# Kernel tuning notes

Hardware: AMD Instinct MI355X
Metric: run time of the kernel (lower is better)

The kernel has to match this reference:

```python
import jax, jax.numpy as jnp
import numpy as np

D_MODEL = 1024
NUM_HEADS = 16
DEPTH = D_MODEL // NUM_HEADS
NEG_INF_SCALE = -1e9


def setup_inputs() -> dict:
    key = jax.random.key(0)
    ks = jax.random.split(key, 12)
    B, S = 2, 2048
    q = jax.random.normal(ks[0], (B, S, D_MODEL), dtype=jnp.float32)
    k = jax.random.normal(ks[1], (B, S, D_MODEL), dtype=jnp.float32)
    v = jax.random.normal(ks[2], (B, S, D_MODEL), dtype=jnp.float32)
    # causal mask: 1 where attention is disallowed (future positions)
    mask = jnp.triu(jnp.ones((S, S), dtype=jnp.float32), k=1)[None, None]
    scale = 1.0 / np.sqrt(D_MODEL)
    Wq = jax.random.normal(ks[3], (D_MODEL, D_MODEL), dtype=jnp.float32) * scale
    bq = jnp.zeros((D_MODEL,), dtype=jnp.float32)
    Wk = jax.random.normal(ks[4], (D_MODEL, D_MODEL), dtype=jnp.float32) * scale
    bk = jnp.zeros((D_MODEL,), dtype=jnp.float32)
    Wv = jax.random.normal(ks[5], (D_MODEL, D_MODEL), dtype=jnp.float32) * scale
    bv = jnp.zeros((D_MODEL,), dtype=jnp.float32)
    Wo = jax.random.normal(ks[6], (D_MODEL, D_MODEL), dtype=jnp.float32) * scale
    bo = jnp.zeros((D_MODEL,), dtype=jnp.float32)
    return {"v": v, "k": k, "q": q, "mask": mask,
            "Wq": Wq, "bq": bq, "Wk": Wk, "bk": bk,
            "Wv": Wv, "bv": bv, "Wo": Wo, "bo": bo}


def _split_heads(x):
    B, S, _ = x.shape
    return x.reshape(B, S, NUM_HEADS, DEPTH).transpose(0, 2, 1, 3)  # [B,H,S,depth]


def reference(v, k, q, mask, Wq, bq, Wk, bk, Wv, bv, Wo, bo):
    B, Sq, _ = q.shape
    qh = _split_heads(q @ Wq + bq)  # [B,H,Sq,depth]
    kh = _split_heads(k @ Wk + bk)  # [B,H,Sk,depth]
    vh = _split_heads(v @ Wv + bv)  # [B,H,Sk,depth]
    logits = jnp.einsum('bhqd,bhkd->bhqk', qh, kh) / jnp.sqrt(
        jnp.asarray(DEPTH, dtype=jnp.float32))
    logits = logits + mask * NEG_INF_SCALE
    attn = jax.nn.softmax(logits, axis=-1)
    out = jnp.einsum('bhqk,bhkd->bhqd', attn, vh)  # [B,H,Sq,depth]
    out = out.transpose(0, 2, 1, 3).reshape(B, Sq, D_MODEL)
    return out @ Wo + bo
```

## Files before the change

### kernel.cpp

```cpp
#include <hip/hip_runtime.h>
#include <stdint.h>

#define D_MODEL 1024
#define NHEADS  16
#define DEPTH   64
#define BATCH   2
#define SEQ     2048
#define M_TOT   (BATCH * SEQ)

#define Q_SCALE 0.18033688011112042f

typedef unsigned short u16;
typedef unsigned int   u32;
typedef __attribute__((ext_vector_type(8))) short bf16x8;
typedef __attribute__((ext_vector_type(4))) float f32x4;

__device__ __forceinline__ float bf2f(unsigned int u) {
    union { unsigned int i; float f; } x;
    x.i = (u & 0xffffu) << 16;
    return x.f;
}
__device__ __forceinline__ u16 f2bf(float f) {
    union { float f; unsigned int i; } x;
    x.f = f;
    unsigned int lsb = (x.i >> 16) & 1u;
    x.i += 0x7fffu + lsb;
    return (u16)(x.i >> 16);
}
__device__ __forceinline__ u32 fbits(float f) {
    union { float f; unsigned int i; } x; x.f = f; return x.i;
}
__device__ __forceinline__ float exp2f_hw(float x) {
    return __builtin_amdgcn_exp2f(x);
}

template <int CTRL>
__device__ __forceinline__ float dppf(float x) {
    int r = __builtin_amdgcn_update_dpp(0, (int)fbits(x), CTRL, 0xF, 0xF, false);
    union { int i; float f; } u; u.i = r; return u.f;
}
__device__ __forceinline__ float redmax16(float x) {
    x = fmaxf(x, dppf<0xB1>(x));
    x = fmaxf(x, dppf<0x4E>(x));
    x = fmaxf(x, dppf<0x124>(x));
    x = fmaxf(x, dppf<0x128>(x));
    return x;
}
__device__ __forceinline__ float redsum16(float x) {
    x += dppf<0xB1>(x);
    x += dppf<0x4E>(x);
    x += dppf<0x124>(x);
    x += dppf<0x128>(x);
    return x;
}

__device__ __forceinline__ void stage16(const u16* g, u16* ldsbase) {
#if __has_builtin(__builtin_amdgcn_global_load_lds)
    __builtin_amdgcn_global_load_lds(
        (const __attribute__((address_space(1))) unsigned int*)g,
        (__attribute__((address_space(3))) unsigned int*)ldsbase, 16, 0, 0);
#else
    int lane = threadIdx.x & 63;
    *(uint4*)(ldsbase + lane * 8) = *(const uint4*)g;
#endif
}

__global__ void sniff_kernel(const u16* __restrict__ q, int* __restrict__ flag) {
    const int t = threadIdx.x;
    int cnt = 0;
    #pragma unroll
    for (int j = 0; j < 4; ++j) {
        unsigned int bits = q[2 * (t + 64 * j)];
        bool susp = ((bits & 0x7fffu) >= 0x4780u);
        cnt += (int)__popcll(__ballot(susp));
    }
    if (t == 0) flag[0] = (cnt >= 32) ? 1 : 0;
}

__global__ __launch_bounds__(256)
void wT_kernel(const void* W0, const void* W1, const void* W2, const void* W3,
               u16* T0, u16* T1, u16* T2, u16* T3, const int* __restrict__ flag) {
    __shared__ u16 t[64][72];
    const int z = blockIdx.z;
    const void* Wv = (z == 0) ? W0 : (z == 1) ? W1 : (z == 2) ? W2 : W3;
    u16* WT = (z == 0) ? T0 : (z == 1) ? T1 : (z == 2) ? T2 : T3;
    const int f32 = *flag;
    const int tid = threadIdx.x;
    const int n0 = blockIdx.x * 64, k0 = blockIdx.y * 64;

    #pragma unroll
    for (int cb = 0; cb < 2; ++cb) {
        int c = tid + cb * 256;
        int kl = c >> 3, nc = (c & 7) * 8;
        size_t off = (size_t)(k0 + kl) * D_MODEL + n0 + nc;
        u16 tmp[8];
        if (f32) {
            const float* W = (const float*)Wv;
            float4 a = *(const float4*)(W + off);
            float4 b = *(const float4*)(W + off + 4);
            tmp[0] = f2bf(a.x); tmp[1] = f2bf(a.y); tmp[2] = f2bf(a.z); tmp[3] = f2bf(a.w);
            tmp[4] = f2bf(b.x); tmp[5] = f2bf(b.y); tmp[6] = f2bf(b.z); tmp[7] = f2bf(b.w);
        } else {
            *(uint4*)tmp = *(const uint4*)((const u16*)Wv + off);
        }
        *(uint4*)&t[kl][nc] = *(uint4*)tmp;
    }
    __syncthreads();
    #pragma unroll
    for (int cb = 0; cb < 2; ++cb) {
        int c = tid + cb * 256;
        int nl = c >> 3, kc = (c & 7) * 8;
        u16 tmp[8];
        #pragma unroll
        for (int i = 0; i < 8; ++i) tmp[i] = t[kc + i][nl];
        *(uint4*)(WT + (size_t)(n0 + nl) * D_MODEL + k0 + kc) = *(uint4*)tmp;
    }
}

struct GemmJob {
    const void* A;
    const u16*  BT;
    const void* bias;
    void*       C;
    int a_ext;
    int cmode;
    float scale;
};

__global__ __launch_bounds__(256)
void gemm5(GemmJob j0, GemmJob j1, GemmJob j2, const int* __restrict__ flag) {
    __shared__ u16 Als[128 * 64];
    __shared__ u16 Bls[128 * 64];
    GemmJob jb = (blockIdx.z == 0) ? j0 : (blockIdx.z == 1) ? j1 : j2;

    const int f32 = *flag;
    const int af32 = jb.a_ext & f32;
    const int tid = threadIdx.x;
    const int w = tid >> 6, lane = tid & 63;
    const int cc = lane & 15, quad = lane >> 4;
    const int wm = w >> 1, wn = w & 1;
    const int m0 = blockIdx.y * 128, n0 = blockIdx.x * 128;

    f32x4 zero4 = {0.f, 0.f, 0.f, 0.f};
    f32x4 acc[4][4];
    #pragma unroll
    for (int i = 0; i < 4; ++i)
        #pragma unroll
        for (int j = 0; j < 4; ++j) acc[i][j] = zero4;

    const int srow_off = lane >> 3;
    const int sg8 = ((lane & 7) ^ ((lane >> 3) & 7)) * 8;

    for (int k0 = 0; k0 < D_MODEL; k0 += 64) {
        __syncthreads();
        #pragma unroll
        for (int i = 0; i < 4; ++i) {
            int c = w * 4 + i;
            int row = c * 8 + srow_off;
            stage16(jb.BT + (size_t)(n0 + row) * D_MODEL + k0 + sg8, &Bls[c * 512]);
        }
        if (!af32) {
            const u16* A = (const u16*)jb.A;
            #pragma unroll
            for (int i = 0; i < 4; ++i) {
                int c = w * 4 + i;
                int row = c * 8 + srow_off;
                stage16(A + (size_t)(m0 + row) * D_MODEL + k0 + sg8, &Als[c * 512]);
            }
        } else {
            const float* A = (const float*)jb.A;
            #pragma unroll
            for (int c2 = 0; c2 < 4; ++c2) {
                int row = c2 * 32 + (tid >> 3);
                int gg = tid & 7;
                int lg = (gg ^ (row & 7)) * 8;
                const float* gp = A + (size_t)(m0 + row) * D_MODEL + k0 + gg * 8;
                float4 a = *(const float4*)gp;
                float4 b = *(const float4*)(gp + 4);
                u16 t8[8];
                t8[0] = f2bf(a.x); t8[1] = f2bf(a.y); t8[2] = f2bf(a.z); t8[3] = f2bf(a.w);
                t8[4] = f2bf(b.x); t8[5] = f2bf(b.y); t8[6] = f2bf(b.z); t8[7] = f2bf(b.w);
                *(uint4*)&Als[row * 64 + lg] = *(uint4*)t8;
            }
        }
        __syncthreads();

        const int sw = cc & 7;
        bf16x8 af[4][2], bf[4][2];
        #pragma unroll
        for (int i = 0; i < 4; ++i) {
            const u16* ar = &Als[(wm * 64 + i * 16 + cc) * 64];
            af[i][0] = *(const bf16x8*)(ar + ((quad ^ sw) * 8));
            af[i][1] = *(const bf16x8*)(ar + (((4 + quad) ^ sw) * 8));
        }
        #pragma unroll
        for (int j = 0; j < 4; ++j) {
            const u16* br = &Bls[(wn * 64 + j * 16 + cc) * 64];
            bf[j][0] = *(const bf16x8*)(br + ((quad ^ sw) * 8));
            bf[j][1] = *(const bf16x8*)(br + (((4 + quad) ^ sw) * 8));
        }
        #pragma unroll
        for (int i = 0; i < 4; ++i)
            #pragma unroll
            for (int j = 0; j < 4; ++j) {
                acc[i][j] = __builtin_amdgcn_mfma_f32_16x16x32_bf16(af[i][0], bf[j][0], acc[i][j], 0, 0, 0);
                acc[i][j] = __builtin_amdgcn_mfma_f32_16x16x32_bf16(af[i][1], bf[j][1], acc[i][j], 0, 0, 0);
            }
    }

    #pragma unroll
    for (int j = 0; j < 4; ++j) {
        int col = n0 + wn * 64 + j * 16 + cc;
        float bv = f32 ? ((const float*)jb.bias)[col] : bf2f(((const u16*)jb.bias)[col]);
        #pragma unroll
        for (int i = 0; i < 4; ++i)
            #pragma unroll
            for (int r = 0; r < 4; ++r) {
                int row = m0 + wm * 64 + i * 16 + quad * 4 + r;
                float vo = (acc[i][j][r] + bv) * jb.scale;
                if (jb.cmode == 0) {
                    ((u16*)jb.C)[(size_t)row * D_MODEL + col] = f2bf(vo);
                } else if (jb.cmode == 1) {
                    int bb = row >> 11, tok = row & (SEQ - 1);
                    int hh = col >> 6, dd = col & 63;
                    int tile = tok >> 6, n = tok & 63;
                    int kap = ((n & 15) << 2) + (n >> 4);
                    ((u16*)jb.C)[((size_t)((bb * NHEADS + hh) * DEPTH + dd)) * SEQ
                                 + tile * 64 + kap] = f2bf(vo);
                } else {
                    if (f32) ((float*)jb.C)[(size_t)row * D_MODEL + col] = vo;
                    else     ((u16*)jb.C)[(size_t)row * D_MODEL + col] = f2bf(vo);
                }
            }
    }
}

__global__ __launch_bounds__(256, 3)
void attn3(const u16* __restrict__ Qp, const u16* __restrict__ Kp,
           const u16* __restrict__ VpT, u16* __restrict__ Ao) {
    __shared__ u16 Kls[2][64 * 64];
    __shared__ u16 Vls[2][64 * 64];
    __shared__ u16 Pls[4][32][72];

    const int tid = threadIdx.x;
    const int w = tid >> 6, lane = tid & 63;
    const int cc = lane & 15, quad = lane >> 4;
    const int qt = (int)(gridDim.x - 1 - blockIdx.x);
    const int h = blockIdx.y, b = blockIdx.z;
    const int qbase = qt * 128 + w * 32;

    bf16x8 qf[2][2];
    #pragma unroll
    for (int mi = 0; mi < 2; ++mi) {
        const u16* qr = Qp + (size_t)(b * SEQ + qbase + mi * 16 + cc) * D_MODEL + h * DEPTH;
        qf[mi][0] = *(const bf16x8*)(qr + quad * 8);
        qf[mi][1] = *(const bf16x8*)(qr + 32 + quad * 8);
    }

    const u16* kbase = Kp + (size_t)(b * SEQ) * D_MODEL + h * DEPTH;
    const u16* vbase = VpT + (size_t)((b * NHEADS + h) * DEPTH) * SEQ;

    const int r8 = lane >> 3;
    const int g8 = ((lane & 7) ^ (r8 & 7)) * 8;

    auto stageKV = [&](int buf, int jt) {
        #pragma unroll
        for (int i = 0; i < 2; ++i) {
            int row = w * 16 + i * 8 + r8;
            stage16(kbase + (size_t)(jt * 64 + row) * D_MODEL + g8,
                    &Kls[buf][(w * 16 + i * 8) * 64]);
            stage16(vbase + (size_t)row * SEQ + jt * 64 + g8,
                    &Vls[buf][(w * 16 + i * 8) * 64]);
        }
    };

    f32x4 zero4 = {0.f, 0.f, 0.f, 0.f};
    f32x4 oacc[2][4];
    #pragma unroll
    for (int mi = 0; mi < 2; ++mi)
        #pragma unroll
        for (int db = 0; db < 4; ++db) oacc[mi][db] = zero4;
    float m_run[2][4], l_run[2][4];
    #pragma unroll
    for (int mi = 0; mi < 2; ++mi)
        #pragma unroll
        for (int r = 0; r < 4; ++r) { m_run[mi][r] = -1e30f; l_run[mi][r] = 0.f; }

    const int jtmax = 2 * qt + 1;
    stageKV(0, 0);

    for (int jt = 0; jt <= jtmax; ++jt) {
        const int cur = jt & 1;
        __syncthreads();
        if (jt < jtmax) stageKV(cur ^ 1, jt + 1);

        if (jt * 64 > qbase + 31) continue;

        const int sw = cc & 7;
        bf16x8 kf[4][2];
        #pragma unroll
        for (int nb = 0; nb < 4; ++nb) {
            const u16* kr = &Kls[cur][(nb * 16 + cc) * 64];
            kf[nb][0] = *(const bf16x8*)(kr + ((quad ^ sw) * 8));
            kf[nb][1] = *(const bf16x8*)(kr + (((4 + quad) ^ sw) * 8));
        }
        f32x4 s[2][4];
        #pragma unroll
        for (int mi = 0; mi < 2; ++mi)
            #pragma unroll
            for (int nb = 0; nb < 4; ++nb) {
                s[mi][nb] = __builtin_amdgcn_mfma_f32_16x16x32_bf16(qf[mi][0], kf[nb][0], zero4, 0, 0, 0);
                s[mi][nb] = __builtin_amdgcn_mfma_f32_16x16x32_bf16(qf[mi][1], kf[nb][1], s[mi][nb], 0, 0, 0);
            }
        #pragma unroll
        for (int mi = 0; mi < 2; ++mi) {
            if (jt * 64 + 63 > qbase + mi * 16) {
                #pragma unroll
                for (int nb = 0; nb < 4; ++nb)
                    #pragma unroll
                    for (int r = 0; r < 4; ++r)
                        if (jt * 64 + nb * 16 + cc > qbase + mi * 16 + quad * 4 + r)
                            s[mi][nb][r] = -1e30f;
            }
        }

        float alpha[2][4];
        #pragma unroll
        for (int mi = 0; mi < 2; ++mi) {
            #pragma unroll
            for (int r = 0; r < 4; ++r) {
                float mrow = redmax16(fmaxf(fmaxf(s[mi][0][r], s[mi][1][r]),
                                            fmaxf(s[mi][2][r], s[mi][3][r])));
                float mn = fmaxf(m_run[mi][r], mrow);
                alpha[mi][r] = exp2f_hw(m_run[mi][r] - mn);
                m_run[mi][r] = mn;
            }
            #pragma unroll
            for (int nb = 0; nb < 4; ++nb)
                #pragma unroll
                for (int r = 0; r < 4; ++r)
                    s[mi][nb][r] = exp2f_hw(s[mi][nb][r] - m_run[mi][r]);
            #pragma unroll
            for (int r = 0; r < 4; ++r)
                l_run[mi][r] = l_run[mi][r] * alpha[mi][r]
                             + ((s[mi][0][r] + s[mi][1][r]) + (s[mi][2][r] + s[mi][3][r]));
            #pragma unroll
            for (int db = 0; db < 4; ++db)
                #pragma unroll
                for (int r = 0; r < 4; ++r)
                    oacc[mi][db][r] *= alpha[mi][r];
        }

        #pragma unroll
        for (int mi = 0; mi < 2; ++mi)
            #pragma unroll
            for (int r = 0; r < 4; ++r) {
                u32 p01 = __builtin_amdgcn_perm(fbits(s[mi][1][r]), fbits(s[mi][0][r]), 0x07060302u);
                u32 p23 = __builtin_amdgcn_perm(fbits(s[mi][3][r]), fbits(s[mi][2][r]), 0x07060302u);
                uint2 pk; pk.x = p01; pk.y = p23;
                *(uint2*)&Pls[w][mi * 16 + quad * 4 + r][4 * cc] = pk;
            }
        __asm__ volatile("" ::: "memory");

        bf16x8 pf[2][2];
        #pragma unroll
        for (int mi = 0; mi < 2; ++mi) {
            pf[mi][0] = *(const bf16x8*)&Pls[w][mi * 16 + cc][quad * 8];
            pf[mi][1] = *(const bf16x8*)&Pls[w][mi * 16 + cc][32 + quad * 8];
        }
        #pragma unroll
        for (int db = 0; db < 4; ++db) {
            const u16* vr = &Vls[cur][(db * 16 + cc) * 64];
            bf16x8 v0 = *(const bf16x8*)(vr + ((quad ^ sw) * 8));
            bf16x8 v1 = *(const bf16x8*)(vr + (((4 + quad) ^ sw) * 8));
            #pragma unroll
            for (int mi = 0; mi < 2; ++mi) {
                oacc[mi][db] = __builtin_amdgcn_mfma_f32_16x16x32_bf16(pf[mi][0], v0, oacc[mi][db], 0, 0, 0);
                oacc[mi][db] = __builtin_amdgcn_mfma_f32_16x16x32_bf16(pf[mi][1], v1, oacc[mi][db], 0, 0, 0);
            }
        }
    }

    #pragma unroll
    for (int mi = 0; mi < 2; ++mi) {
        float linv[4];
        #pragma unroll
        for (int r = 0; r < 4; ++r) linv[r] = 1.0f / redsum16(l_run[mi][r]);
        #pragma unroll
        for (int db = 0; db < 4; ++db)
            #pragma unroll
            for (int r = 0; r < 4; ++r) {
                size_t row = (size_t)(b * SEQ + qbase + mi * 16 + quad * 4 + r);
                Ao[row * D_MODEL + h * DEPTH + db * 16 + cc] =
                    f2bf(oacc[mi][db][r] * linv[r]);
            }
    }
}

extern "C" void kernel_launch(void* const* d_in, const int* in_sizes, int n_in,
                              void* d_out, int out_size, void* d_ws, size_t ws_size,
                              hipStream_t stream) {
    const void* v  = d_in[0];
    const void* k  = d_in[1];
    const void* q  = d_in[2];
    const void* Wq = d_in[4];
    const void* bq = d_in[5];
    const void* Wk = d_in[6];
    const void* bk = d_in[7];
    const void* Wv = d_in[8];
    const void* bv = d_in[9];
    const void* Wo = d_in[10];
    const void* bo = d_in[11];

    char* base = (char*)d_ws;
    int* flag = (int*)base;
    const size_t WSZ = (size_t)D_MODEL * D_MODEL;
    const size_t TOK = (size_t)M_TOT * D_MODEL;
    u16* WqT = (u16*)(base + 256);
    u16* WkT = WqT + WSZ;
    u16* WvT = WkT + WSZ;
    u16* WoT = WvT + WSZ;
    u16* Qp  = WoT + WSZ;
    u16* Kp  = Qp + TOK;
    u16* VpT = Kp + TOK;
    u16* Ao  = VpT + TOK;

    sniff_kernel<<<1, 64, 0, stream>>>((const u16*)q, flag);

    wT_kernel<<<dim3(16, 16, 4), 256, 0, stream>>>(Wq, Wk, Wv, Wo,
                                                   WqT, WkT, WvT, WoT, flag);

    GemmJob jq = {q,  WqT, bq, Qp,    1, 0, Q_SCALE};
    GemmJob jk = {k,  WkT, bk, Kp,    1, 0, 1.0f};
    GemmJob jv = {v,  WvT, bv, VpT,   1, 1, 1.0f};
    gemm5<<<dim3(8, 32, 3), 256, 0, stream>>>(jq, jk, jv, flag);

    attn3<<<dim3(16, 16, 2), 256, 0, stream>>>(Qp, Kp, VpT, Ao);

    GemmJob jo = {Ao, WoT, bo, d_out, 0, 2, 1.0f};
    gemm5<<<dim3(8, 32, 1), 256, 0, stream>>>(jo, jo, jo, flag);
}
```

Baseline: 303.8 us.

## Pre-convert activations to bf16 and remap GEMM blocks per XCD

Adds a separate conversion kernel that turns the fp32 q/k/v inputs into bf16 buffers, so the projection GEMM can always stage A tiles with async direct-to-LDS loads instead of converting fp32 to bf16 in registers. The GEMM block index is also remapped so that blocks landing on the same XCD share M rows across all N tiles, which should improve L2 reuse. The cost is an extra full pass over the inputs (reading fp32, writing bf16) plus more workspace, with the attention output buffer now aliased onto Qb.

```diff
diff --git a/kernel.cpp b/kernel.cpp
--- a/kernel.cpp
+++ b/kernel.cpp
@@ -75,6 +75,27 @@
         cnt += (int)__popcll(__ballot(susp));
     }
     if (t == 0) flag[0] = (cnt >= 32) ? 1 : 0;
+}
+
+__global__ __launch_bounds__(256)
+void conv_kernel(const void* s0, const void* s1, const void* s2,
+                 u16* d0, u16* d1, u16* d2, const int* __restrict__ flag) {
+    const int z = blockIdx.z;
+    const void* src = (z == 0) ? s0 : (z == 1) ? s1 : s2;
+    u16* dst = (z == 0) ? d0 : (z == 1) ? d1 : d2;
+    const int f32 = *flag;
+    const size_t i = ((size_t)blockIdx.x * 256 + threadIdx.x) * 8;
+    if (f32) {
+        const float* s = (const float*)src + i;
+        float4 a = *(const float4*)s;
+        float4 b = *(const float4*)(s + 4);
+        u16 t8[8];
+        t8[0] = f2bf(a.x); t8[1] = f2bf(a.y); t8[2] = f2bf(a.z); t8[3] = f2bf(a.w);
+        t8[4] = f2bf(b.x); t8[5] = f2bf(b.y); t8[6] = f2bf(b.z); t8[7] = f2bf(b.w);
+        *(uint4*)(dst + i) = *(uint4*)t8;
+    } else {
+        *(uint4*)(dst + i) = *(const uint4*)((const u16*)src + i);
+    }
 }
 
 __global__ __launch_bounds__(256)
@@ -118,28 +139,34 @@
 }
 
 struct GemmJob {
-    const void* A;
+    const u16*  A;
     const u16*  BT;
     const void* bias;
     void*       C;
-    int a_ext;
     int cmode;
     float scale;
 };
 
 __global__ __launch_bounds__(256)
-void gemm5(GemmJob j0, GemmJob j1, GemmJob j2, const int* __restrict__ flag) {
+void gemm6(GemmJob j0, GemmJob j1, GemmJob j2, const int* __restrict__ flag) {
     __shared__ u16 Als[128 * 64];
     __shared__ u16 Bls[128 * 64];
-    GemmJob jb = (blockIdx.z == 0) ? j0 : (blockIdx.z == 1) ? j1 : j2;
+
+    const u32 lin = blockIdx.x + gridDim.x * (blockIdx.y + gridDim.y * blockIdx.z);
+    const u32 xcd = lin & 7, idx = lin >> 3;
+    const u32 per = (gridDim.y * gridDim.z) >> 3;
+    const u32 mz = xcd * per + (idx >> 3);
+    const u32 nb_ = idx & 7;
+    const u32 zz = mz / gridDim.y;
+    const u32 my = mz % gridDim.y;
+    GemmJob jb = (zz == 0) ? j0 : (zz == 1) ? j1 : j2;
 
     const int f32 = *flag;
-    const int af32 = jb.a_ext & f32;
     const int tid = threadIdx.x;
     const int w = tid >> 6, lane = tid & 63;
     const int cc = lane & 15, quad = lane >> 4;
     const int wm = w >> 1, wn = w & 1;
-    const int m0 = blockIdx.y * 128, n0 = blockIdx.x * 128;
+    const int m0 = my * 128, n0 = nb_ * 128;
 
     f32x4 zero4 = {0.f, 0.f, 0.f, 0.f};
     f32x4 acc[4][4];
@@ -158,30 +185,7 @@
             int c = w * 4 + i;
             int row = c * 8 + srow_off;
             stage16(jb.BT + (size_t)(n0 + row) * D_MODEL + k0 + sg8, &Bls[c * 512]);
-        }
-        if (!af32) {
-            const u16* A = (const u16*)jb.A;
-            #pragma unroll
-            for (int i = 0; i < 4; ++i) {
-                int c = w * 4 + i;
-                int row = c * 8 + srow_off;
-                stage16(A + (size_t)(m0 + row) * D_MODEL + k0 + sg8, &Als[c * 512]);
-            }
-        } else {
-            const float* A = (const float*)jb.A;
-            #pragma unroll
-            for (int c2 = 0; c2 < 4; ++c2) {
-                int row = c2 * 32 + (tid >> 3);
-                int gg = tid & 7;
-                int lg = (gg ^ (row & 7)) * 8;
-                const float* gp = A + (size_t)(m0 + row) * D_MODEL + k0 + gg * 8;
-                float4 a = *(const float4*)gp;
-                float4 b = *(const float4*)(gp + 4);
-                u16 t8[8];
-                t8[0] = f2bf(a.x); t8[1] = f2bf(a.y); t8[2] = f2bf(a.z); t8[3] = f2bf(a.w);
-                t8[4] = f2bf(b.x); t8[5] = f2bf(b.y); t8[6] = f2bf(b.z); t8[7] = f2bf(b.w);
-                *(uint4*)&Als[row * 64 + lg] = *(uint4*)t8;
-            }
+            stage16(jb.A  + (size_t)(m0 + row) * D_MODEL + k0 + sg8, &Als[c * 512]);
         }
         __syncthreads();
 
@@ -420,23 +424,27 @@
     u16* WkT = WqT + WSZ;
     u16* WvT = WkT + WSZ;
     u16* WoT = WvT + WSZ;
-    u16* Qp  = WoT + WSZ;
+    u16* Qb  = WoT + WSZ;
+    u16* Kb  = Qb + TOK;
+    u16* Vb  = Kb + TOK;
+    u16* Qp  = Vb + TOK;
     u16* Kp  = Qp + TOK;
     u16* VpT = Kp + TOK;
-    u16* Ao  = VpT + TOK;
+    u16* Ao  = Qb;
 
     sniff_kernel<<<1, 64, 0, stream>>>((const u16*)q, flag);
 
+    conv_kernel<<<dim3(2048, 1, 3), 256, 0, stream>>>(q, k, v, Qb, Kb, Vb, flag);
     wT_kernel<<<dim3(16, 16, 4), 256, 0, stream>>>(Wq, Wk, Wv, Wo,
                                                    WqT, WkT, WvT, WoT, flag);
 
-    GemmJob jq = {q,  WqT, bq, Qp,    1, 0, Q_SCALE};
-    GemmJob jk = {k,  WkT, bk, Kp,    1, 0, 1.0f};
-    GemmJob jv = {v,  WvT, bv, VpT,   1, 1, 1.0f};
-    gemm5<<<dim3(8, 32, 3), 256, 0, stream>>>(jq, jk, jv, flag);
+    GemmJob jq = {Qb, WqT, bq, Qp,    0, Q_SCALE};
+    GemmJob jk = {Kb, WkT, bk, Kp,    0, 1.0f};
+    GemmJob jv = {Vb, WvT, bv, VpT,   1, 1.0f};
+    gemm6<<<dim3(8, 32, 3), 256, 0, stream>>>(jq, jk, jv, flag);
 
     attn3<<<dim3(16, 16, 2), 256, 0, stream>>>(Qp, Kp, VpT, Ao);
 
-    GemmJob jo = {Ao, WoT, bo, d_out, 0, 2, 1.0f};
-    gemm5<<<dim3(8, 32, 1), 256, 0, stream>>>(jo, jo, jo, flag);
-}
+    GemmJob jo = {Ao, WoT, bo, d_out, 2, 1.0f};
+    gemm6<<<dim3(8, 32, 1), 256, 0, stream>>>(jo, jo, jo, flag);
+}
```

After: 299.5 us. Within noise of the previous version (-1.4%).
